# Optimization experiments

Measured on AMD Instinct MI355X. Metric: run time of the kernel, lower is better.

The kernel has to match this reference:

```python
import jax, jax.numpy as jnp
import numpy as np

L, C, K, V, G, T, NC, CIN = 9, 256, 3, 25, 9, 128, 60, 3


def _ln(x, w, b, axes, eps=1e-5):
    # LayerNorm over (channels, joints) per time step, affine params broadcast over time
    m = x.mean(axes, keepdims=True)
    v = x.var(axes, keepdims=True)
    return (x - m) * jax.lax.rsqrt(v + eps) * w + b


def setup_inputs() -> dict:
    key = jax.random.key(0)
    ks = jax.random.split(key, 8)
    s = 0.02  # weight init scale
    return {
        "x": jax.random.normal(ks[0], (1, CIN, T, V), jnp.float32),
        "A": jax.random.uniform(ks[1], (K, V, V), jnp.float32),
        "ln_in_w": jnp.ones((CIN, V), jnp.float32),
        "ln_in_b": jnp.zeros((CIN, V), jnp.float32),
        "W_in": jax.random.normal(ks[2], (C, CIN), jnp.float32) * s,
        "b_in": jnp.zeros((C,), jnp.float32),
        "Wg": jax.random.normal(ks[3], (L, K * C, C), jnp.float32) * s,
        "bg": jnp.zeros((L, K * C), jnp.float32),
        "ln1_w": jnp.ones((L, C, V), jnp.float32),
        "ln1_b": jnp.zeros((L, C, V), jnp.float32),
        "Wt": jax.random.normal(ks[4], (L, C, C, G), jnp.float32) * s,
        "bt": jnp.zeros((L, C), jnp.float32),
        "ln2_w": jnp.ones((L, C, V), jnp.float32),
        "ln2_b": jnp.zeros((L, C, V), jnp.float32),
        "imp": jnp.ones((L, K, V, V), jnp.float32),
        "W_out": jax.random.normal(ks[5], (NC, C), jnp.float32) * s,
        "b_out": jnp.zeros((NC,), jnp.float32),
    }


def reference(x, A, ln_in_w, ln_in_b, W_in, b_in, Wg, bg, ln1_w, ln1_b,
              Wt, bt, ln2_w, ln2_b, imp, W_out, b_out):
    ghalf = G // 2
    Al = A[None] * imp                      # (L, K, V, V) edge-importance weighted adjacency
    xs = x[0].transpose(1, 0, 2)            # (T, CIN, V): stream frames
    fifo0 = jnp.zeros((L, C, G, V), x.dtype)

    def step(carry, xt):
        fifo, fifo_res = carry
        # input LayerNorm + 1x1 conv (fcn_in)
        h = _ln(xt, ln_in_w, ln_in_b, (0, 1))
        h = jnp.einsum('oc,cv->ov', W_in, h) + b_in[:, None]   # (C, V)
        new_f, new_fr = [], []
        for l in range(L):
            res = h                                             # identity residual (in==out, stride==1)
            # graph conv: 1x1 conv -> (K, C, V), einsum with partitioned adjacency
            y = (jnp.einsum('oc,cv->ov', Wg[l], h) + bg[l][:, None]).reshape(K, C, V)
            z = jnp.einsum('kcv,kvw->cw', y, Al[l])             # (C, V)
            # FIFO shift: newest frame at time index 0
            f = jnp.concatenate([z[:, None, :], fifo[l, :, :-1]], axis=1)      # (C, G, V)
            fr = jnp.concatenate([res[:, None, :], fifo_res[l, :, :-1]], axis=1)
            # tcn: LN -> ReLU -> temporal conv (G,1) -> LN
            a = jax.nn.relu(_ln(f, ln1_w[l][:, None, :], ln1_b[l][:, None, :], (0, 2)))
            t = jnp.einsum('ocg,cgv->ov', Wt[l], a) + bt[l][:, None]           # (C, V)
            t = _ln(t, ln2_w[l], ln2_b[l], (0, 1))
            # residual from center of residual FIFO, then ReLU
            h = jax.nn.relu(t + fr[:, ghalf])
            new_f.append(f)
            new_fr.append(fr)
        pooled = h.mean(axis=1)                                 # avg_pool2d over (T=1, V)
        logits = W_out @ pooled + b_out                         # (NC,)
        return (jnp.stack(new_f), jnp.stack(new_fr)), logits

    _, out = jax.lax.scan(step, (fifo0, fifo0), xs)
    return out  # (T, NC): per-frame class logits
```

## Files before the change

kernel.cpp:

```cpp
#include <hip/hip_runtime.h>

#define TT  128
#define CC  256
#define VV  25
#define KK  3
#define GG  9
#define LL  9
#define NCC 60
#define CINN 3
#define TV    (TT*VV)
#define N4    4096
#define KDIM2 (CC*GG)
#define UR    ((TT+8)*32)
#define YSTR  104
#define HSTR  264

typedef __attribute__((ext_vector_type(8))) short bf16x8;
typedef __attribute__((ext_vector_type(4))) float f32x4;
typedef unsigned short us16;

__device__ __forceinline__ us16 f2bf(float f) {
    union { float f; unsigned u; } a; a.f = f;
    unsigned r = a.u + 0x7fff + ((a.u >> 16) & 1);
    return (us16)(r >> 16);
}
__device__ __forceinline__ float bf2f(us16 u) {
    union { unsigned u; float f; } a; a.u = ((unsigned)u) << 16; return a.f;
}
__device__ __forceinline__ bf16x8 ld8(const us16* p) { return *(const bf16x8*)p; }


#define PN1 (LL*KK*CC*CC)
#define PN2 (LL*CC*CC*GG)
#define PN3 (LL*KK*32*32)
#define PN4 (LL*CC*32)
#define PTOT (PN1+PN2+PN3+PN4)

__global__ void k_prep(const float* __restrict__ Wg, const float* __restrict__ Wt,
                       const float* __restrict__ A, const float* __restrict__ imp,
                       const float* __restrict__ bg,
                       us16* __restrict__ Wgb, us16* __restrict__ Wt2b,
                       us16* __restrict__ AlTb, float* __restrict__ bgAl) {
    int i = blockIdx.x * 256 + threadIdx.x;
    if (i < PN1) {
        Wgb[i] = f2bf(Wg[i]);
    } else if (i < PN1 + PN2) {
        int j = i - PN1;
        int kk = j % (CC*GG);
        int o  = (j / (CC*GG)) % CC;
        int l  = j / (CC*CC*GG);
        int g = kk >> 8, c = kk & 255;
        Wt2b[j] = f2bf(Wt[((size_t)(l*CC + o)*CC + c)*GG + g]);
    } else if (i < PN1 + PN2 + PN3) {
        int j = i - PN1 - PN2;
        int v = j & 31, w = (j >> 5) & 31;
        int lk = j >> 10, k = lk % KK, l = lk / KK;
        float val = 0.f;
        if (v < VV && w < VV)
            val = A[(k*VV+v)*VV + w] * imp[((size_t)(l*KK+k)*VV+v)*VV + w];
        AlTb[j] = f2bf(val);
    } else if (i < PTOT) {
        int j = i - PN1 - PN2 - PN3;
        int w = j & 31, c = (j >> 5) & 255, l = j >> 13;
        float s = 0.f;
        if (w < VV) {
            for (int k = 0; k < KK; k++) {
                float col = 0.f;
                for (int v = 0; v < VV; v++)
                    col += A[(k*VV+v)*VV + w] * imp[((size_t)(l*KK+k)*VV+v)*VV + w];
                s += bg[l*KK*CC + k*CC + c] * col;
            }
        }
        bgAl[j] = s;
    }
}


__device__ __forceinline__ void blk_reduce2(float& s, float& q, float* red) {
    #pragma unroll
    for (int off = 32; off; off >>= 1) {
        s += __shfl_down(s, off);
        q += __shfl_down(q, off);
    }
    int lane = threadIdx.x & 63, w = threadIdx.x >> 6;
    if (lane == 0) { red[w] = s; red[4+w] = q; }
    __syncthreads();
    s = red[0]+red[1]+red[2]+red[3];
    q = red[4]+red[5]+red[6]+red[7];
}


template<int FIRST>
__global__ __launch_bounds__(256, 1) void k_gcn(
    const float* __restrict__ x, const float* __restrict__ lniw,
    const float* __restrict__ lnib, const float* __restrict__ Win,
    const float* __restrict__ bin,
    const us16* __restrict__ Tt, const float* __restrict__ btv,
    const float* __restrict__ ln2w, const float* __restrict__ ln2b,
    const us16* __restrict__ HresidTb,
    const us16* __restrict__ Wgb,
    const us16* __restrict__ AlTb, const float* __restrict__ bgAl,
    const float* __restrict__ lnw, const float* __restrict__ lnb,
    us16* __restrict__ HTb, us16* __restrict__ Ut2) {

    const int t = blockIdx.x, tid = threadIdx.x;
    if (t >= TT) {
        int tp = t - TT, c = tid;
        #pragma unroll
        for (int w = 0; w < 32; w++) {
            float u = (w < VV) ? fmaxf(lnb[c*VV + w], 0.f) : 0.f;
            Ut2[(size_t)(tp*32 + w)*CC + c] = f2bf(u);
        }
        return;
    }
    __shared__ __align__(16) us16 Yt[CC*YSTR];
    __shared__ __align__(16) us16 sH[32*HSTR];
    __shared__ float red[8];
    __shared__ float sx[80];
    __shared__ float sh[80];
    const int wave = tid >> 6, lane = tid & 63, quad = lane >> 4, l16 = lane & 15;

    if (FIRST) {
        if (tid < CINN*VV)
            sx[tid] = x[(size_t)(tid/VV)*TV + t*VV + (tid%VV)];
        __syncthreads();
        float s = 0.f, q = 0.f;
        for (int i = 0; i < CINN*VV; i++) { float v = sx[i]; s += v; q += v*v; }
        float m  = s * (1.f/75.f);
        float var = q * (1.f/75.f) - m*m;
        float rs = rsqrtf(var + 1e-5f);
        if (tid < CINN*VV)
            sh[tid] = (sx[tid]-m)*rs*lniw[tid] + lnib[tid];
        __syncthreads();
        int c = tid;
        float w0 = Win[c*3+0], w1 = Win[c*3+1], w2 = Win[c*3+2], bb = bin[c];
        #pragma unroll
        for (int v = 0; v < VV; v++) {
            float acc = bb + w0*sh[v] + w1*sh[VV+v] + w2*sh[2*VV+v];
            us16 b = f2bf(acc);
            HTb[(size_t)(t*32 + v)*CC + c] = b;
            sH[v*HSTR + c] = b;
        }
        #pragma unroll
        for (int v = VV; v < 32; v++)
            sH[v*HSTR + c] = 0;
        __syncthreads();
    } else {
        int c = tid;
        float btc = btv[c];
        float vals[VV];
        float s = 0.f, q = 0.f;
        #pragma unroll
        for (int v = 0; v < VV; v++) {
            float xv = bf2f(Tt[(size_t)(t*32 + v)*CC + c]) + btc;
            vals[v] = xv; s += xv; q += xv*xv;
        }
        blk_reduce2(s, q, red);
        float m = s * (1.f/6400.f);
        float var = q * (1.f/6400.f) - m*m;
        float rs = rsqrtf(var + 1e-5f);
        #pragma unroll
        for (int v = 0; v < VV; v++) {
            float res = (t >= 4) ? bf2f(HresidTb[(size_t)((t-4)*32 + v)*CC + c]) : 0.f;
            float o = fmaxf((vals[v]-m)*rs*ln2w[c*VV+v] + ln2b[c*VV+v] + res, 0.f);
            us16 b = f2bf(o);
            HTb[(size_t)(t*32 + v)*CC + c] = b;
            sH[v*HSTR + c] = b;
        }
        #pragma unroll
        for (int v = VV; v < 32; v++)
            sH[v*HSTR + c] = 0;
        __syncthreads();
    }

    bf16x8 al[2][3];
    #pragma unroll
    for (int nt = 0; nt < 2; nt++)
        #pragma unroll
        for (int s = 0; s < 3; s++)
            al[nt][s] = ld8(AlTb + (size_t)(s*32 + nt*16 + l16)*32 + quad*8);

    bf16x8 bf[2][8];
    #pragma unroll
    for (int nt = 0; nt < 2; nt++)
        #pragma unroll
        for (int s = 0; s < 8; s++)
            bf[nt][s] = *(const bf16x8*)(sH + (nt*16 + l16)*HSTR + s*32 + quad*8);

    bf16x8 wA0,wA1,wA2,wA3,wA4,wA5,wA6,wA7;
    bf16x8 wB0,wB1,wB2,wB3,wB4,wB5,wB6,wB7;
    bf16x8 wC0,wC1,wC2,wC3,wC4,wC5,wC6,wC7;

#define PLD(S, mtv) { \
    const us16* ap_ = Wgb + (size_t)(wave*192 + (mtv)*16 + l16)*CC + quad*8; \
    S##0 = ld8(ap_);       S##1 = ld8(ap_ + 32); \
    S##2 = ld8(ap_ + 64);  S##3 = ld8(ap_ + 96); \
    S##4 = ld8(ap_ + 128); S##5 = ld8(ap_ + 160); \
    S##6 = ld8(ap_ + 192); S##7 = ld8(ap_ + 224); }
#define PMFW(S, mtv) { \
    f32x4 p0a = {}, p0b = {}, p1a = {}, p1b = {}; \
    p0a = __builtin_amdgcn_mfma_f32_16x16x32_bf16(S##0, bf[0][0], p0a,0,0,0); \
    p1a = __builtin_amdgcn_mfma_f32_16x16x32_bf16(S##0, bf[1][0], p1a,0,0,0); \
    p0b = __builtin_amdgcn_mfma_f32_16x16x32_bf16(S##1, bf[0][1], p0b,0,0,0); \
    p1b = __builtin_amdgcn_mfma_f32_16x16x32_bf16(S##1, bf[1][1], p1b,0,0,0); \
    p0a = __builtin_amdgcn_mfma_f32_16x16x32_bf16(S##2, bf[0][2], p0a,0,0,0); \
    p1a = __builtin_amdgcn_mfma_f32_16x16x32_bf16(S##2, bf[1][2], p1a,0,0,0); \
    p0b = __builtin_amdgcn_mfma_f32_16x16x32_bf16(S##3, bf[0][3], p0b,0,0,0); \
    p1b = __builtin_amdgcn_mfma_f32_16x16x32_bf16(S##3, bf[1][3], p1b,0,0,0); \
    p0a = __builtin_amdgcn_mfma_f32_16x16x32_bf16(S##4, bf[0][4], p0a,0,0,0); \
    p1a = __builtin_amdgcn_mfma_f32_16x16x32_bf16(S##4, bf[1][4], p1a,0,0,0); \
    p0b = __builtin_amdgcn_mfma_f32_16x16x32_bf16(S##5, bf[0][5], p0b,0,0,0); \
    p1b = __builtin_amdgcn_mfma_f32_16x16x32_bf16(S##5, bf[1][5], p1b,0,0,0); \
    p0a = __builtin_amdgcn_mfma_f32_16x16x32_bf16(S##6, bf[0][6], p0a,0,0,0); \
    p1a = __builtin_amdgcn_mfma_f32_16x16x32_bf16(S##6, bf[1][6], p1a,0,0,0); \
    p0b = __builtin_amdgcn_mfma_f32_16x16x32_bf16(S##7, bf[0][7], p0b,0,0,0); \
    p1b = __builtin_amdgcn_mfma_f32_16x16x32_bf16(S##7, bf[1][7], p1b,0,0,0); \
    int mb_ = wave*192 + (mtv)*16 + quad*4; \
    _Pragma("unroll") \
    for (int r_ = 0; r_ < 4; r_++) { \
        int m_ = mb_ + r_; \
        int base_ = (m_ & 255)*YSTR + (m_ >> 8)*32 + l16; \
        Yt[base_]      = f2bf(p0a[r_] + p0b[r_]); \
        Yt[base_ + 16] = f2bf(p1a[r_] + p1b[r_]); \
    } }

    PLD(wA, 0); PLD(wB, 1); PLD(wC, 2);
    #pragma unroll 1
    for (int mt = 0; mt < 9; mt += 3) {
        PMFW(wA, mt);     PLD(wA, mt + 3);
        PMFW(wB, mt + 1); PLD(wB, mt + 4);
        PMFW(wC, mt + 2); PLD(wC, mt + 5);
    }
    PMFW(wA, 9); PMFW(wB, 10); PMFW(wC, 11);
#undef PLD
#undef PMFW
    __syncthreads();

    f32x4 z[4][2];
    #pragma unroll
    for (int mt = 0; mt < 4; mt++) { z[mt][0] = (f32x4){}; z[mt][1] = (f32x4){}; }
    #pragma unroll
    for (int mt = 0; mt < 4; mt++)
        #pragma unroll
        for (int s = 0; s < 3; s++) {
            bf16x8 a = *(const bf16x8*)(Yt + (wave*64 + mt*16 + l16)*YSTR + s*32 + quad*8);
            z[mt][0] = __builtin_amdgcn_mfma_f32_16x16x32_bf16(a, al[0][s], z[mt][0], 0,0,0);
            z[mt][1] = __builtin_amdgcn_mfma_f32_16x16x32_bf16(a, al[1][s], z[mt][1], 0,0,0);
        }

    float s_ = 0.f, q_ = 0.f;
    #pragma unroll
    for (int mt = 0; mt < 4; mt++)
        #pragma unroll
        for (int nt = 0; nt < 2; nt++)
            #pragma unroll
            for (int r = 0; r < 4; r++) {
                int c = wave*64 + mt*16 + quad*4 + r;
                int w = nt*16 + l16;
                float zb = z[mt][nt][r] + bgAl[c*32 + w];
                z[mt][nt][r] = zb;
                if (w < VV) { s_ += zb; q_ += zb*zb; }
            }
    blk_reduce2(s_, q_, red);
    float m = s_ * (1.f/6400.f);
    float var = q_ * (1.f/6400.f) - m*m;
    float rs = rsqrtf(var + 1e-5f);
    #pragma unroll
    for (int mt = 0; mt < 4; mt++)
        #pragma unroll
        for (int nt = 0; nt < 2; nt++) {
            int w = nt*16 + l16;
            if (w < VV) {
                int c0 = wave*64 + mt*16 + quad*4;
                ushort4 pk;
                float u0 = fmaxf((z[mt][nt][0]-m)*rs*lnw[(c0+0)*VV+w] + lnb[(c0+0)*VV+w], 0.f);
                float u1 = fmaxf((z[mt][nt][1]-m)*rs*lnw[(c0+1)*VV+w] + lnb[(c0+1)*VV+w], 0.f);
                float u2 = fmaxf((z[mt][nt][2]-m)*rs*lnw[(c0+2)*VV+w] + lnb[(c0+2)*VV+w], 0.f);
                float u3 = fmaxf((z[mt][nt][3]-m)*rs*lnw[(c0+3)*VV+w] + lnb[(c0+3)*VV+w], 0.f);
                pk.x = f2bf(u0); pk.y = f2bf(u1); pk.z = f2bf(u2); pk.w = f2bf(u3);
                *(ushort4*)(Ut2 + (size_t)((t+8)*32 + w)*CC + c0) = pk;
            }
        }
    #pragma unroll
    for (int r = VV; r < 32; r++)
        Ut2[(size_t)((t+8)*32 + r)*CC + tid] = 0;
}


__global__ __launch_bounds__(256) void k_gemm2(const us16* __restrict__ A,
                                               const us16* __restrict__ Ut2,
                                               us16* __restrict__ Tt) {
    __shared__ us16 TL[64*72];
    const int tid = threadIdx.x;
    const int wave = tid >> 6, lane = tid & 63, quad = lane >> 4, l16 = lane & 15;
    const int bid = blockIdx.x;
    const int xcd = bid & 7, grp = bid >> 3;
    const int mt = (xcd >> 2)*2 + (grp & 1);
    const int nt = (xcd & 3)*16 + (grp >> 1);
    const int m0b = mt*64, n0b = nt*64;
    const int m0w = m0b + (wave & 1)*32;
    const int n0w = n0b + (wave >> 1)*32;
    const us16* ap = A + (size_t)(m0w + l16)*KDIM2 + quad*8;
    f32x4 acc00 = {}, acc01 = {}, acc10 = {}, acc11 = {};
    bf16x8 aA0,aA1,bA0,bA1, aB0,aB1,bB0,bB1, aC0,aC1,bC0,bC1, aD0,aD1,bD0,bD1;

#define GLD(S, it) { \
    int k0 = (it)*32; \
    a##S##0 = ld8(ap + k0); \
    a##S##1 = ld8(ap + k0 + 16*KDIM2); \
    int g = k0 >> 8; \
    const us16* bp = Ut2 + (size_t)(n0w + (8-g)*32 + l16)*CC + (k0 & 255) + quad*8; \
    b##S##0 = ld8(bp); \
    b##S##1 = ld8(bp + 16*CC); }
#define GMF(S) { \
    acc00 = __builtin_amdgcn_mfma_f32_16x16x32_bf16(a##S##0, b##S##0, acc00,0,0,0); \
    acc01 = __builtin_amdgcn_mfma_f32_16x16x32_bf16(a##S##0, b##S##1, acc01,0,0,0); \
    acc10 = __builtin_amdgcn_mfma_f32_16x16x32_bf16(a##S##1, b##S##0, acc10,0,0,0); \
    acc11 = __builtin_amdgcn_mfma_f32_16x16x32_bf16(a##S##1, b##S##1, acc11,0,0,0); }

    GLD(A, 0); GLD(B, 1); GLD(C, 2); GLD(D, 3);
    #pragma unroll 1
    for (int it = 4; it <= KDIM2/32 - 4; it += 4) {
        GMF(A); GLD(A, it);
        GMF(B); GLD(B, it+1);
        GMF(C); GLD(C, it+2);
        GMF(D); GLD(D, it+3);
    }
    GMF(A); GMF(B); GMF(C); GMF(D);
#undef GLD
#undef GMF

    #pragma unroll
    for (int r = 0; r < 4; r++) {
        int mlo = (wave & 1)*32 + quad*4 + r;
        int nlo = (wave >> 1)*32 + l16;
        TL[nlo*72 + mlo]           = f2bf(acc00[r]);
        TL[(nlo+16)*72 + mlo]      = f2bf(acc01[r]);
        TL[nlo*72 + mlo + 16]      = f2bf(acc10[r]);
        TL[(nlo+16)*72 + mlo + 16] = f2bf(acc11[r]);
    }
    __syncthreads();
    #pragma unroll
    for (int u = 0; u < 2; u++) {
        int q2 = tid + u*256;
        int row = q2 >> 3, ch = q2 & 7;
        *(bf16x8*)(Tt + (size_t)(n0b + row)*CC + m0b + ch*8) =
            *(const bf16x8*)(TL + row*72 + ch*8);
    }
}


__global__ __launch_bounds__(256) void k_fin(const us16* __restrict__ Tt,
                                             const us16* __restrict__ HresidTb,
                                             const float* __restrict__ btv,
                                             const float* __restrict__ lnw,
                                             const float* __restrict__ lnb,
                                             const float* __restrict__ Wout,
                                             const float* __restrict__ bout,
                                             float* __restrict__ out) {
    int t = blockIdx.x, tid = threadIdx.x;
    __shared__ float red[8];
    __shared__ float sp[CC];
    int c = tid;
    float btc = btv[c];
    float vals[VV];
    float s = 0.f, q = 0.f;
    #pragma unroll
    for (int v = 0; v < VV; v++) {
        float xv = bf2f(Tt[(size_t)(t*32 + v)*CC + c]) + btc;
        vals[v] = xv; s += xv; q += xv*xv;
    }
    blk_reduce2(s, q, red);
    float m = s * (1.f/6400.f);
    float var = q * (1.f/6400.f) - m*m;
    float rs = rsqrtf(var + 1e-5f);
    float pl = 0.f;
    #pragma unroll
    for (int v = 0; v < VV; v++) {
        float res = (t >= 4) ? bf2f(HresidTb[(size_t)((t-4)*32 + v)*CC + c]) : 0.f;
        float o = fmaxf((vals[v]-m)*rs*lnw[c*VV+v] + lnb[c*VV+v] + res, 0.f);
        pl += o;
    }
    sp[c] = pl * (1.f/VV);
    __syncthreads();
    if (tid < NCC) {
        float a = bout[tid];
        for (int cc = 0; cc < CC; cc++) a = fmaf(Wout[tid*CC+cc], sp[cc], a);
        out[t*NCC + tid] = a;
    }
}


extern "C" void kernel_launch(void* const* d_in, const int* in_sizes, int n_in,
                              void* d_out, int out_size, void* d_ws, size_t ws_size,
                              hipStream_t stream) {
    const float* x    = (const float*)d_in[0];
    const float* A    = (const float*)d_in[1];
    const float* lniw = (const float*)d_in[2];
    const float* lnib = (const float*)d_in[3];
    const float* Win  = (const float*)d_in[4];
    const float* bin  = (const float*)d_in[5];
    const float* Wg   = (const float*)d_in[6];
    const float* bg   = (const float*)d_in[7];
    const float* ln1w = (const float*)d_in[8];
    const float* ln1b = (const float*)d_in[9];
    const float* Wt   = (const float*)d_in[10];
    const float* bt   = (const float*)d_in[11];
    const float* ln2w = (const float*)d_in[12];
    const float* ln2b = (const float*)d_in[13];
    const float* imp  = (const float*)d_in[14];
    const float* Wout = (const float*)d_in[15];
    const float* bout = (const float*)d_in[16];
    float* out = (float*)d_out;

    float* ws = (float*)d_ws;
    size_t off = 0;
    auto alloc = [&](size_t n) { float* p = ws + off; off += (n + 255) & ~(size_t)255; return p; };
    float* bgAl = alloc((size_t)LL*CC*32);
    us16* HTb0 = (us16*)alloc((size_t)TT*32*CC/2);
    us16* HTb1 = (us16*)alloc((size_t)TT*32*CC/2);
    us16* Tt   = (us16*)alloc((size_t)N4*CC/2);
    us16* Wgb  = (us16*)alloc((size_t)LL*KK*CC*CC/2);
    us16* Wt2b = (us16*)alloc((size_t)LL*CC*KDIM2/2);
    us16* Ut2  = (us16*)alloc((size_t)UR*CC/2);
    us16* AlTb = (us16*)alloc((size_t)LL*KK*32*32/2);
    (void)ws_size; (void)in_sizes; (void)n_in; (void)out_size;

    k_prep<<<(PTOT + 255)/256, 256, 0, stream>>>(Wg, Wt, A, imp, bg,
                                                 Wgb, Wt2b, AlTb, bgAl);

    us16* hPrev = HTb0; us16* hNext = HTb1;
    for (int l = 0; l < LL; l++) {
        if (l == 0) {
            k_gcn<1><<<TT + 8, 256, 0, stream>>>(
                x, lniw, lnib, Win, bin,
                Tt, bt, ln2w, ln2b, hPrev,
                Wgb, AlTb, bgAl, ln1w, ln1b,
                hPrev , Ut2);
        } else {
            k_gcn<0><<<TT + 8, 256, 0, stream>>>(
                x, lniw, lnib, Win, bin,
                Tt, bt + (size_t)(l-1)*CC,
                ln2w + (size_t)(l-1)*CC*VV, ln2b + (size_t)(l-1)*CC*VV,
                hPrev ,
                Wgb + (size_t)l*KK*CC*CC,
                AlTb + (size_t)l*KK*32*32, bgAl + (size_t)l*CC*32,
                ln1w + (size_t)l*CC*VV, ln1b + (size_t)l*CC*VV,
                hNext , Ut2);
            us16* tmp = hPrev; hPrev = hNext; hNext = tmp;
        }
        k_gemm2<<<256, 256, 0, stream>>>(
            Wt2b + (size_t)l*CC*KDIM2, Ut2, Tt);
    }
    k_fin<<<TT, 256, 0, stream>>>(Tt, hPrev,
        bt + (size_t)(LL-1)*CC, ln2w + (size_t)(LL-1)*CC*VV, ln2b + (size_t)(LL-1)*CC*VV,
        Wout, bout, out);
}
```

Before: 712.5 us.

## Fuse temporal conv GEMM with next layer's graph conv into per-frame kernel

Replaces the separate temporal-conv GEMM kernel and the following gcn kernel with a single per-frame kernel of 512 threads. Each frame block computes its own Wt·U GEMM over the 9 FIFO taps with double-buffered LDS staging, then applies LN2, the residual, the next layer's graph conv and LN1 in place. U buffers are ping-ponged so layers can read and write without conflict. This roughly halves launch count and drops the Tt round trip through global memory. In exchange, each block re-reads the full Wt weights per frame with no cross-frame reuse, and only 136 blocks run.

```diff
diff --git a/kernel.cpp b/kernel.cpp
--- a/kernel.cpp
+++ b/kernel.cpp
@@ -9,11 +9,11 @@
 #define NCC 60
 #define CINN 3
 #define TV    (TT*VV)
-#define N4    4096
 #define KDIM2 (CC*GG)
 #define UR    ((TT+8)*32)
 #define YSTR  104
 #define HSTR  264
+#define BSTR  260
 
 typedef __attribute__((ext_vector_type(8))) short bf16x8;
 typedef __attribute__((ext_vector_type(4))) float f32x4;
@@ -28,6 +28,22 @@
     union { unsigned u; float f; } a; a.u = ((unsigned)u) << 16; return a.f;
 }
 __device__ __forceinline__ bf16x8 ld8(const us16* p) { return *(const bf16x8*)p; }
+
+
+template<int NW>
+__device__ __forceinline__ void blk_reduce2t(float& s, float& q, float* red) {
+    #pragma unroll
+    for (int off = 32; off; off >>= 1) {
+        s += __shfl_down(s, off);
+        q += __shfl_down(q, off);
+    }
+    int lane = threadIdx.x & 63, w = threadIdx.x >> 6;
+    if (lane == 0) { red[w] = s; red[NW + w] = q; }
+    __syncthreads();
+    s = 0.f; q = 0.f;
+    #pragma unroll
+    for (int i = 0; i < NW; i++) { s += red[i]; q += red[NW + i]; }
+}
 
 
 #define PN1 (LL*KK*CC*CC)
@@ -76,30 +92,12 @@
 }
 
 
-__device__ __forceinline__ void blk_reduce2(float& s, float& q, float* red) {
-    #pragma unroll
-    for (int off = 32; off; off >>= 1) {
-        s += __shfl_down(s, off);
-        q += __shfl_down(q, off);
-    }
-    int lane = threadIdx.x & 63, w = threadIdx.x >> 6;
-    if (lane == 0) { red[w] = s; red[4+w] = q; }
-    __syncthreads();
-    s = red[0]+red[1]+red[2]+red[3];
-    q = red[4]+red[5]+red[6]+red[7];
-}
-
-
-template<int FIRST>
-__global__ __launch_bounds__(256, 1) void k_gcn(
+__global__ __launch_bounds__(256, 1) void k_gcn0(
     const float* __restrict__ x, const float* __restrict__ lniw,
     const float* __restrict__ lnib, const float* __restrict__ Win,
     const float* __restrict__ bin,
-    const us16* __restrict__ Tt, const float* __restrict__ btv,
-    const float* __restrict__ ln2w, const float* __restrict__ ln2b,
-    const us16* __restrict__ HresidTb,
-    const us16* __restrict__ Wgb,
-    const us16* __restrict__ AlTb, const float* __restrict__ bgAl,
+    const us16* __restrict__ Wgb0,
+    const us16* __restrict__ AlTb0, const float* __restrict__ bgAl0,
     const float* __restrict__ lnw, const float* __restrict__ lnb,
     us16* __restrict__ HTb, us16* __restrict__ Ut2) {
 
@@ -120,10 +118,10 @@
     __shared__ float sh[80];
     const int wave = tid >> 6, lane = tid & 63, quad = lane >> 4, l16 = lane & 15;
 
-    if (FIRST) {
-        if (tid < CINN*VV)
-            sx[tid] = x[(size_t)(tid/VV)*TV + t*VV + (tid%VV)];
-        __syncthreads();
+    if (tid < CINN*VV)
+        sx[tid] = x[(size_t)(tid/VV)*TV + t*VV + (tid%VV)];
+    __syncthreads();
+    {
         float s = 0.f, q = 0.f;
         for (int i = 0; i < CINN*VV; i++) { float v = sx[i]; s += v; q += v*v; }
         float m  = s * (1.f/75.f);
@@ -131,7 +129,9 @@
         float rs = rsqrtf(var + 1e-5f);
         if (tid < CINN*VV)
             sh[tid] = (sx[tid]-m)*rs*lniw[tid] + lnib[tid];
-        __syncthreads();
+    }
+    __syncthreads();
+    {
         int c = tid;
         float w0 = Win[c*3+0], w1 = Win[c*3+1], w2 = Win[c*3+2], bb = bin[c];
         #pragma unroll
@@ -144,41 +144,15 @@
         #pragma unroll
         for (int v = VV; v < 32; v++)
             sH[v*HSTR + c] = 0;
-        __syncthreads();
-    } else {
-        int c = tid;
-        float btc = btv[c];
-        float vals[VV];
-        float s = 0.f, q = 0.f;
-        #pragma unroll
-        for (int v = 0; v < VV; v++) {
-            float xv = bf2f(Tt[(size_t)(t*32 + v)*CC + c]) + btc;
-            vals[v] = xv; s += xv; q += xv*xv;
-        }
-        blk_reduce2(s, q, red);
-        float m = s * (1.f/6400.f);
-        float var = q * (1.f/6400.f) - m*m;
-        float rs = rsqrtf(var + 1e-5f);
-        #pragma unroll
-        for (int v = 0; v < VV; v++) {
-            float res = (t >= 4) ? bf2f(HresidTb[(size_t)((t-4)*32 + v)*CC + c]) : 0.f;
-            float o = fmaxf((vals[v]-m)*rs*ln2w[c*VV+v] + ln2b[c*VV+v] + res, 0.f);
-            us16 b = f2bf(o);
-            HTb[(size_t)(t*32 + v)*CC + c] = b;
-            sH[v*HSTR + c] = b;
-        }
-        #pragma unroll
-        for (int v = VV; v < 32; v++)
-            sH[v*HSTR + c] = 0;
-        __syncthreads();
-    }
+    }
+    __syncthreads();
 
     bf16x8 al[2][3];
     #pragma unroll
     for (int nt = 0; nt < 2; nt++)
         #pragma unroll
         for (int s = 0; s < 3; s++)
-            al[nt][s] = ld8(AlTb + (size_t)(s*32 + nt*16 + l16)*32 + quad*8);
+            al[nt][s] = ld8(AlTb0 + (size_t)(s*32 + nt*16 + l16)*32 + quad*8);
 
     bf16x8 bf[2][8];
     #pragma unroll
@@ -192,7 +166,7 @@
     bf16x8 wC0,wC1,wC2,wC3,wC4,wC5,wC6,wC7;
 
 #define PLD(S, mtv) { \
-    const us16* ap_ = Wgb + (size_t)(wave*192 + (mtv)*16 + l16)*CC + quad*8; \
+    const us16* ap_ = Wgb0 + (size_t)(wave*192 + (mtv)*16 + l16)*CC + quad*8; \
     S##0 = ld8(ap_);       S##1 = ld8(ap_ + 32); \
     S##2 = ld8(ap_ + 64);  S##3 = ld8(ap_ + 96); \
     S##4 = ld8(ap_ + 128); S##5 = ld8(ap_ + 160); \
@@ -243,9 +217,9 @@
     for (int mt = 0; mt < 4; mt++)
         #pragma unroll
         for (int s = 0; s < 3; s++) {
-            bf16x8 a = *(const bf16x8*)(Yt + (wave*64 + mt*16 + l16)*YSTR + s*32 + quad*8);
-            z[mt][0] = __builtin_amdgcn_mfma_f32_16x16x32_bf16(a, al[0][s], z[mt][0], 0,0,0);
-            z[mt][1] = __builtin_amdgcn_mfma_f32_16x16x32_bf16(a, al[1][s], z[mt][1], 0,0,0);
+            bf16x8 av = *(const bf16x8*)(Yt + (wave*64 + mt*16 + l16)*YSTR + s*32 + quad*8);
+            z[mt][0] = __builtin_amdgcn_mfma_f32_16x16x32_bf16(av, al[0][s], z[mt][0], 0,0,0);
+            z[mt][1] = __builtin_amdgcn_mfma_f32_16x16x32_bf16(av, al[1][s], z[mt][1], 0,0,0);
         }
 
     float s_ = 0.f, q_ = 0.f;
@@ -257,11 +231,11 @@
             for (int r = 0; r < 4; r++) {
                 int c = wave*64 + mt*16 + quad*4 + r;
                 int w = nt*16 + l16;
-                float zb = z[mt][nt][r] + bgAl[c*32 + w];
+                float zb = z[mt][nt][r] + bgAl0[c*32 + w];
                 z[mt][nt][r] = zb;
                 if (w < VV) { s_ += zb; q_ += zb*zb; }
             }
-    blk_reduce2(s_, q_, red);
+    blk_reduce2t<4>(s_, q_, red);
     float m = s_ * (1.f/6400.f);
     float var = q_ * (1.f/6400.f) - m*m;
     float rs = rsqrtf(var + 1e-5f);
@@ -287,106 +261,260 @@
 }
 
 
-__global__ __launch_bounds__(256) void k_gemm2(const us16* __restrict__ A,
-                                               const us16* __restrict__ Ut2,
-                                               us16* __restrict__ Tt) {
-    __shared__ us16 TL[64*72];
-    const int tid = threadIdx.x;
+template<int FIN>
+__global__ __launch_bounds__(512, 1) void k_layer(
+    const us16* __restrict__ Awt,
+    const float* __restrict__ btv, const float* __restrict__ l2w,
+    const float* __restrict__ l2b,
+    const us16* __restrict__ HTprev, const us16* __restrict__ Uin,
+    const us16* __restrict__ WgbL, const us16* __restrict__ AlTbL,
+    const float* __restrict__ bgAlL,
+    const float* __restrict__ lnwL, const float* __restrict__ lnbL,
+    us16* __restrict__ HTout, us16* __restrict__ Uout,
+    const float* __restrict__ Wout, const float* __restrict__ bout,
+    float* __restrict__ out) {
+
+    const int t = blockIdx.x, tid = threadIdx.x;
+    __shared__ __align__(16) us16 Yt[CC*YSTR];
+    __shared__ __align__(16) us16 sH[32*HSTR];
+    __shared__ float red[16];
     const int wave = tid >> 6, lane = tid & 63, quad = lane >> 4, l16 = lane & 15;
-    const int bid = blockIdx.x;
-    const int xcd = bid & 7, grp = bid >> 3;
-    const int mt = (xcd >> 2)*2 + (grp & 1);
-    const int nt = (xcd & 3)*16 + (grp >> 1);
-    const int m0b = mt*64, n0b = nt*64;
-    const int m0w = m0b + (wave & 1)*32;
-    const int n0w = n0b + (wave >> 1)*32;
-    const us16* ap = A + (size_t)(m0w + l16)*KDIM2 + quad*8;
+
+    if (FIN == 0 && t >= TT) {
+        if (tid < CC) {
+            int tp = t - TT, c = tid;
+            #pragma unroll
+            for (int w = 0; w < 32; w++) {
+                float u = (w < VV) ? fmaxf(lnbL[c*VV + w], 0.f) : 0.f;
+                Uout[(size_t)(tp*32 + w)*CC + c] = f2bf(u);
+            }
+        }
+        return;
+    }
+
+    us16* Bst = Yt;
+    const us16* ap = Awt + (size_t)(wave*32 + l16)*KDIM2 + quad*8;
     f32x4 acc00 = {}, acc01 = {}, acc10 = {}, acc11 = {};
-    bf16x8 aA0,aA1,bA0,bA1, aB0,aB1,bB0,bB1, aC0,aC1,bC0,bC1, aD0,aD1,bD0,bD1;
-
-#define GLD(S, it) { \
-    int k0 = (it)*32; \
-    a##S##0 = ld8(ap + k0); \
-    a##S##1 = ld8(ap + k0 + 16*KDIM2); \
-    int g = k0 >> 8; \
-    const us16* bp = Ut2 + (size_t)(n0w + (8-g)*32 + l16)*CC + (k0 & 255) + quad*8; \
-    b##S##0 = ld8(bp); \
-    b##S##1 = ld8(bp + 16*CC); }
-#define GMF(S) { \
-    acc00 = __builtin_amdgcn_mfma_f32_16x16x32_bf16(a##S##0, b##S##0, acc00,0,0,0); \
-    acc01 = __builtin_amdgcn_mfma_f32_16x16x32_bf16(a##S##0, b##S##1, acc01,0,0,0); \
-    acc10 = __builtin_amdgcn_mfma_f32_16x16x32_bf16(a##S##1, b##S##0, acc10,0,0,0); \
-    acc11 = __builtin_amdgcn_mfma_f32_16x16x32_bf16(a##S##1, b##S##1, acc11,0,0,0); }
-
-    GLD(A, 0); GLD(B, 1); GLD(C, 2); GLD(D, 3);
+    const int brow = tid >> 4, bcol = (tid & 15) * 16;
+    const us16* ubase = Uin + (size_t)((t+8)*32 + brow)*CC + bcol;
+    {
+        bf16x8 b0 = ld8(ubase), b1 = ld8(ubase + 8);
+        *(bf16x8*)(Bst + brow*BSTR + bcol)     = b0;
+        *(bf16x8*)(Bst + brow*BSTR + bcol + 8) = b1;
+    }
+    __syncthreads();
     #pragma unroll 1
-    for (int it = 4; it <= KDIM2/32 - 4; it += 4) {
-        GMF(A); GLD(A, it);
-        GMF(B); GLD(B, it+1);
-        GMF(C); GLD(C, it+2);
-        GMF(D); GLD(D, it+3);
-    }
-    GMF(A); GMF(B); GMF(C); GMF(D);
-#undef GLD
-#undef GMF
-
-    #pragma unroll
-    for (int r = 0; r < 4; r++) {
-        int mlo = (wave & 1)*32 + quad*4 + r;
-        int nlo = (wave >> 1)*32 + l16;
-        TL[nlo*72 + mlo]           = f2bf(acc00[r]);
-        TL[(nlo+16)*72 + mlo]      = f2bf(acc01[r]);
-        TL[nlo*72 + mlo + 16]      = f2bf(acc10[r]);
-        TL[(nlo+16)*72 + mlo + 16] = f2bf(acc11[r]);
-    }
-    __syncthreads();
-    #pragma unroll
-    for (int u = 0; u < 2; u++) {
-        int q2 = tid + u*256;
-        int row = q2 >> 3, ch = q2 & 7;
-        *(bf16x8*)(Tt + (size_t)(n0b + row)*CC + m0b + ch*8) =
-            *(const bf16x8*)(TL + row*72 + ch*8);
-    }
-}
-
-
-__global__ __launch_bounds__(256) void k_fin(const us16* __restrict__ Tt,
-                                             const us16* __restrict__ HresidTb,
-                                             const float* __restrict__ btv,
-                                             const float* __restrict__ lnw,
-                                             const float* __restrict__ lnb,
-                                             const float* __restrict__ Wout,
-                                             const float* __restrict__ bout,
-                                             float* __restrict__ out) {
-    int t = blockIdx.x, tid = threadIdx.x;
-    __shared__ float red[8];
-    __shared__ float sp[CC];
-    int c = tid;
-    float btc = btv[c];
+    for (int g = 0; g < 9; g++) {
+        const us16* apg = ap + g*256;
+        bf16x8 aL[8], aH[8];
+        #pragma unroll
+        for (int s = 0; s < 8; s++) {
+            aL[s] = ld8(apg + s*32);
+            aH[s] = ld8(apg + 16*KDIM2 + s*32);
+        }
+        bf16x8 bn0 = {}, bn1 = {};
+        if (g < 8) {
+            const us16* un = ubase - (size_t)(g+1)*32*CC;
+            bn0 = ld8(un); bn1 = ld8(un + 8);
+        }
+        const us16* bb = Bst + (g & 1)*(32*BSTR);
+        #pragma unroll
+        for (int s = 0; s < 8; s++) {
+            bf16x8 b0 = *(const bf16x8*)(bb + l16*BSTR + s*32 + quad*8);
+            bf16x8 b1 = *(const bf16x8*)(bb + (l16+16)*BSTR + s*32 + quad*8);
+            acc00 = __builtin_amdgcn_mfma_f32_16x16x32_bf16(aL[s], b0, acc00,0,0,0);
+            acc01 = __builtin_amdgcn_mfma_f32_16x16x32_bf16(aL[s], b1, acc01,0,0,0);
+            acc10 = __builtin_amdgcn_mfma_f32_16x16x32_bf16(aH[s], b0, acc10,0,0,0);
+            acc11 = __builtin_amdgcn_mfma_f32_16x16x32_bf16(aH[s], b1, acc11,0,0,0);
+        }
+        __syncthreads();
+        if (g < 8) {
+            us16* bw = Bst + ((g+1) & 1)*(32*BSTR) + brow*BSTR + bcol;
+            *(bf16x8*)bw       = bn0;
+            *(bf16x8*)(bw + 8) = bn1;
+        }
+        __syncthreads();
+    }
+
+    #pragma unroll
+    for (int mh = 0; mh < 2; mh++)
+        #pragma unroll
+        for (int nh = 0; nh < 2; nh++) {
+            f32x4 av = (mh == 0) ? (nh == 0 ? acc00 : acc01)
+                                 : (nh == 0 ? acc10 : acc11);
+            int v = l16 + nh*16;
+            int cb = wave*32 + quad*4 + mh*16;
+            #pragma unroll
+            for (int r = 0; r < 4; r += 2) {
+                ushort2 p;
+                p.x = f2bf(av[r]); p.y = f2bf(av[r+1]);
+                *(ushort2*)(sH + v*HSTR + cb + r) = p;
+            }
+        }
+    __syncthreads();
+
     float vals[VV];
-    float s = 0.f, q = 0.f;
-    #pragma unroll
-    for (int v = 0; v < VV; v++) {
-        float xv = bf2f(Tt[(size_t)(t*32 + v)*CC + c]) + btc;
-        vals[v] = xv; s += xv; q += xv*xv;
-    }
-    blk_reduce2(s, q, red);
-    float m = s * (1.f/6400.f);
-    float var = q * (1.f/6400.f) - m*m;
+    float s_ = 0.f, q_ = 0.f;
+    if (tid < CC) {
+        float btc = btv[tid];
+        #pragma unroll
+        for (int v = 0; v < VV; v++) {
+            float xv = bf2f(sH[v*HSTR + tid]) + btc;
+            vals[v] = xv; s_ += xv; q_ += xv*xv;
+        }
+    }
+    blk_reduce2t<8>(s_, q_, red);
+    float m = s_ * (1.f/6400.f);
+    float var = q_ * (1.f/6400.f) - m*m;
     float rs = rsqrtf(var + 1e-5f);
-    float pl = 0.f;
-    #pragma unroll
-    for (int v = 0; v < VV; v++) {
-        float res = (t >= 4) ? bf2f(HresidTb[(size_t)((t-4)*32 + v)*CC + c]) : 0.f;
-        float o = fmaxf((vals[v]-m)*rs*lnw[c*VV+v] + lnb[c*VV+v] + res, 0.f);
-        pl += o;
-    }
-    sp[c] = pl * (1.f/VV);
-    __syncthreads();
-    if (tid < NCC) {
-        float a = bout[tid];
-        for (int cc = 0; cc < CC; cc++) a = fmaf(Wout[tid*CC+cc], sp[cc], a);
-        out[t*NCC + tid] = a;
+
+    if (FIN == 1) {
+        float* sp = (float*)Yt;
+        if (tid < CC) {
+            int c = tid;
+            float pl = 0.f;
+            #pragma unroll
+            for (int v = 0; v < VV; v++) {
+                float res = (t >= 4) ? bf2f(HTprev[(size_t)((t-4)*32 + v)*CC + c]) : 0.f;
+                float o = fmaxf((vals[v]-m)*rs*l2w[c*VV+v] + l2b[c*VV+v] + res, 0.f);
+                pl += o;
+            }
+            sp[c] = pl * (1.f/VV);
+        }
+        __syncthreads();
+        if (tid < NCC) {
+            float acc = bout[tid];
+            for (int cc = 0; cc < CC; cc++) acc = fmaf(Wout[tid*CC+cc], sp[cc], acc);
+            out[t*NCC + tid] = acc;
+        }
+        return;
+    }
+
+    if (tid < CC) {
+        int c = tid;
+        #pragma unroll
+        for (int v = 0; v < VV; v++) {
+            float res = (t >= 4) ? bf2f(HTprev[(size_t)((t-4)*32 + v)*CC + c]) : 0.f;
+            float o = fmaxf((vals[v]-m)*rs*l2w[c*VV+v] + l2b[c*VV+v] + res, 0.f);
+            us16 b = f2bf(o);
+            HTout[(size_t)(t*32 + v)*CC + c] = b;
+            sH[v*HSTR + c] = b;
+        }
+        #pragma unroll
+        for (int v = VV; v < 32; v++)
+            sH[v*HSTR + c] = 0;
+    }
+    __syncthreads();
+
+    bf16x8 al[2][3];
+    #pragma unroll
+    for (int nt = 0; nt < 2; nt++)
+        #pragma unroll
+        for (int s = 0; s < 3; s++)
+            al[nt][s] = ld8(AlTbL + (size_t)(s*32 + nt*16 + l16)*32 + quad*8);
+
+    bf16x8 bf[2][8];
+    #pragma unroll
+    for (int nt = 0; nt < 2; nt++)
+        #pragma unroll
+        for (int s = 0; s < 8; s++)
+            bf[nt][s] = *(const bf16x8*)(sH + (nt*16 + l16)*HSTR + s*32 + quad*8);
+
+    bf16x8 wA0,wA1,wA2,wA3,wA4,wA5,wA6,wA7;
+    bf16x8 wB0,wB1,wB2,wB3,wB4,wB5,wB6,wB7;
+    bf16x8 wC0,wC1,wC2,wC3,wC4,wC5,wC6,wC7;
+
+#define PLD(S, mtv) { \
+    const us16* ap_ = WgbL + (size_t)(wave*96 + (mtv)*16 + l16)*CC + quad*8; \
+    S##0 = ld8(ap_);       S##1 = ld8(ap_ + 32); \
+    S##2 = ld8(ap_ + 64);  S##3 = ld8(ap_ + 96); \
+    S##4 = ld8(ap_ + 128); S##5 = ld8(ap_ + 160); \
+    S##6 = ld8(ap_ + 192); S##7 = ld8(ap_ + 224); }
+#define PMFW(S, mtv) { \
+    f32x4 p0a = {}, p0b = {}, p1a = {}, p1b = {}; \
+    p0a = __builtin_amdgcn_mfma_f32_16x16x32_bf16(S##0, bf[0][0], p0a,0,0,0); \
+    p1a = __builtin_amdgcn_mfma_f32_16x16x32_bf16(S##0, bf[1][0], p1a,0,0,0); \
+    p0b = __builtin_amdgcn_mfma_f32_16x16x32_bf16(S##1, bf[0][1], p0b,0,0,0); \
+    p1b = __builtin_amdgcn_mfma_f32_16x16x32_bf16(S##1, bf[1][1], p1b,0,0,0); \
+    p0a = __builtin_amdgcn_mfma_f32_16x16x32_bf16(S##2, bf[0][2], p0a,0,0,0); \
+    p1a = __builtin_amdgcn_mfma_f32_16x16x32_bf16(S##2, bf[1][2], p1a,0,0,0); \
+    p0b = __builtin_amdgcn_mfma_f32_16x16x32_bf16(S##3, bf[0][3], p0b,0,0,0); \
+    p1b = __builtin_amdgcn_mfma_f32_16x16x32_bf16(S##3, bf[1][3], p1b,0,0,0); \
+    p0a = __builtin_amdgcn_mfma_f32_16x16x32_bf16(S##4, bf[0][4], p0a,0,0,0); \
+    p1a = __builtin_amdgcn_mfma_f32_16x16x32_bf16(S##4, bf[1][4], p1a,0,0,0); \
+    p0b = __builtin_amdgcn_mfma_f32_16x16x32_bf16(S##5, bf[0][5], p0b,0,0,0); \
+    p1b = __builtin_amdgcn_mfma_f32_16x16x32_bf16(S##5, bf[1][5], p1b,0,0,0); \
+    p0a = __builtin_amdgcn_mfma_f32_16x16x32_bf16(S##6, bf[0][6], p0a,0,0,0); \
+    p1a = __builtin_amdgcn_mfma_f32_16x16x32_bf16(S##6, bf[1][6], p1a,0,0,0); \
+    p0b = __builtin_amdgcn_mfma_f32_16x16x32_bf16(S##7, bf[0][7], p0b,0,0,0); \
+    p1b = __builtin_amdgcn_mfma_f32_16x16x32_bf16(S##7, bf[1][7], p1b,0,0,0); \
+    int mb_ = wave*96 + (mtv)*16 + quad*4; \
+    _Pragma("unroll") \
+    for (int r_ = 0; r_ < 4; r_++) { \
+        int m_ = mb_ + r_; \
+        int base_ = (m_ & 255)*YSTR + (m_ >> 8)*32 + l16; \
+        Yt[base_]      = f2bf(p0a[r_] + p0b[r_]); \
+        Yt[base_ + 16] = f2bf(p1a[r_] + p1b[r_]); \
+    } }
+
+    PLD(wA, 0); PLD(wB, 1); PLD(wC, 2);
+    PMFW(wA, 0); PLD(wA, 3);
+    PMFW(wB, 1); PLD(wB, 4);
+    PMFW(wC, 2); PLD(wC, 5);
+    PMFW(wA, 3); PMFW(wB, 4); PMFW(wC, 5);
+#undef PLD
+#undef PMFW
+    __syncthreads();
+
+    f32x4 z[2][2];
+    z[0][0] = (f32x4){}; z[0][1] = (f32x4){};
+    z[1][0] = (f32x4){}; z[1][1] = (f32x4){};
+    #pragma unroll
+    for (int mt = 0; mt < 2; mt++)
+        #pragma unroll
+        for (int s = 0; s < 3; s++) {
+            bf16x8 av = *(const bf16x8*)(Yt + (wave*32 + mt*16 + l16)*YSTR + s*32 + quad*8);
+            z[mt][0] = __builtin_amdgcn_mfma_f32_16x16x32_bf16(av, al[0][s], z[mt][0], 0,0,0);
+            z[mt][1] = __builtin_amdgcn_mfma_f32_16x16x32_bf16(av, al[1][s], z[mt][1], 0,0,0);
+        }
+
+    float su = 0.f, qu = 0.f;
+    #pragma unroll
+    for (int mt = 0; mt < 2; mt++)
+        #pragma unroll
+        for (int nt = 0; nt < 2; nt++)
+            #pragma unroll
+            for (int r = 0; r < 4; r++) {
+                int c = wave*32 + mt*16 + quad*4 + r;
+                int w = nt*16 + l16;
+                float zb = z[mt][nt][r] + bgAlL[c*32 + w];
+                z[mt][nt][r] = zb;
+                if (w < VV) { su += zb; qu += zb*zb; }
+            }
+    blk_reduce2t<8>(su, qu, red);
+    float mu = su * (1.f/6400.f);
+    float vu = qu * (1.f/6400.f) - mu*mu;
+    float ru = rsqrtf(vu + 1e-5f);
+    #pragma unroll
+    for (int mt = 0; mt < 2; mt++)
+        #pragma unroll
+        for (int nt = 0; nt < 2; nt++) {
+            int w = nt*16 + l16;
+            if (w < VV) {
+                int c0 = wave*32 + mt*16 + quad*4;
+                ushort4 pk;
+                float u0 = fmaxf((z[mt][nt][0]-mu)*ru*lnwL[(c0+0)*VV+w] + lnbL[(c0+0)*VV+w], 0.f);
+                float u1 = fmaxf((z[mt][nt][1]-mu)*ru*lnwL[(c0+1)*VV+w] + lnbL[(c0+1)*VV+w], 0.f);
+                float u2 = fmaxf((z[mt][nt][2]-mu)*ru*lnwL[(c0+2)*VV+w] + lnbL[(c0+2)*VV+w], 0.f);
+                float u3 = fmaxf((z[mt][nt][3]-mu)*ru*lnwL[(c0+3)*VV+w] + lnbL[(c0+3)*VV+w], 0.f);
+                pk.x = f2bf(u0); pk.y = f2bf(u1); pk.z = f2bf(u2); pk.w = f2bf(u3);
+                *(ushort4*)(Uout + (size_t)((t+8)*32 + w)*CC + c0) = pk;
+            }
+        }
+    if (tid < CC) {
+        #pragma unroll
+        for (int r = VV; r < 32; r++)
+            Uout[(size_t)((t+8)*32 + r)*CC + tid] = 0;
     }
 }
 
@@ -419,40 +547,40 @@
     float* bgAl = alloc((size_t)LL*CC*32);
     us16* HTb0 = (us16*)alloc((size_t)TT*32*CC/2);
     us16* HTb1 = (us16*)alloc((size_t)TT*32*CC/2);
-    us16* Tt   = (us16*)alloc((size_t)N4*CC/2);
     us16* Wgb  = (us16*)alloc((size_t)LL*KK*CC*CC/2);
     us16* Wt2b = (us16*)alloc((size_t)LL*CC*KDIM2/2);
-    us16* Ut2  = (us16*)alloc((size_t)UR*CC/2);
+    us16* UA   = (us16*)alloc((size_t)UR*CC/2);
+    us16* UB   = (us16*)alloc((size_t)UR*CC/2);
     us16* AlTb = (us16*)alloc((size_t)LL*KK*32*32/2);
     (void)ws_size; (void)in_sizes; (void)n_in; (void)out_size;
 
     k_prep<<<(PTOT + 255)/256, 256, 0, stream>>>(Wg, Wt, A, imp, bg,
                                                  Wgb, Wt2b, AlTb, bgAl);
 
-    us16* hPrev = HTb0; us16* hNext = HTb1;
-    for (int l = 0; l < LL; l++) {
-        if (l == 0) {
-            k_gcn<1><<<TT + 8, 256, 0, stream>>>(
-                x, lniw, lnib, Win, bin,
-                Tt, bt, ln2w, ln2b, hPrev,
-                Wgb, AlTb, bgAl, ln1w, ln1b,
-                hPrev , Ut2);
-        } else {
-            k_gcn<0><<<TT + 8, 256, 0, stream>>>(
-                x, lniw, lnib, Win, bin,
-                Tt, bt + (size_t)(l-1)*CC,
-                ln2w + (size_t)(l-1)*CC*VV, ln2b + (size_t)(l-1)*CC*VV,
-                hPrev ,
-                Wgb + (size_t)l*KK*CC*CC,
-                AlTb + (size_t)l*KK*32*32, bgAl + (size_t)l*CC*32,
-                ln1w + (size_t)l*CC*VV, ln1b + (size_t)l*CC*VV,
-                hNext , Ut2);
-            us16* tmp = hPrev; hPrev = hNext; hNext = tmp;
-        }
-        k_gemm2<<<256, 256, 0, stream>>>(
-            Wt2b + (size_t)l*CC*KDIM2, Ut2, Tt);
-    }
-    k_fin<<<TT, 256, 0, stream>>>(Tt, hPrev,
-        bt + (size_t)(LL-1)*CC, ln2w + (size_t)(LL-1)*CC*VV, ln2b + (size_t)(LL-1)*CC*VV,
+    k_gcn0<<<TT + 8, 256, 0, stream>>>(x, lniw, lnib, Win, bin,
+                                       Wgb, AlTb, bgAl, ln1w, ln1b,
+                                       HTb0, UA);
+
+    us16* Ubuf[2] = { UA, UB };
+    us16* Hbuf[2] = { HTb0, HTb1 };
+    for (int l = 1; l <= 8; l++) {
+        k_layer<0><<<TT + 8, 512, 0, stream>>>(
+            Wt2b + (size_t)(l-1)*CC*KDIM2,
+            bt + (size_t)(l-1)*CC,
+            ln2w + (size_t)(l-1)*CC*VV, ln2b + (size_t)(l-1)*CC*VV,
+            Hbuf[(l-1) & 1], Ubuf[(l-1) & 1],
+            Wgb + (size_t)l*KK*CC*CC,
+            AlTb + (size_t)l*KK*32*32, bgAl + (size_t)l*CC*32,
+            ln1w + (size_t)l*CC*VV, ln1b + (size_t)l*CC*VV,
+            Hbuf[l & 1], Ubuf[l & 1],
+            nullptr, nullptr, nullptr);
+    }
+    k_layer<1><<<TT, 512, 0, stream>>>(
+        Wt2b + (size_t)8*CC*KDIM2,
+        bt + (size_t)8*CC,
+        ln2w + (size_t)8*CC*VV, ln2b + (size_t)8*CC*VV,
+        Hbuf[0], Ubuf[0],
+        nullptr, nullptr, nullptr, nullptr, nullptr,
+        nullptr, nullptr,
         Wout, bout, out);
 }
```

New measurement: 783.7 us. 10.0% more time.
